# Performance work log

Hardware: AMD Instinct MI355X
Metric: run time of the kernel (lower is better)

Reference implementation:

```python
import math
import jax, jax.numpy as jnp
import numpy as np

PATCH_NUMS = (1, 2, 3, 4, 5, 6, 8, 10, 13, 16)
_lens = [p * p for p in PATCH_NUMS]
_cum = np.concatenate([[0], np.cumsum(_lens)])
BEGIN_ENDS = [(int(_cum[i]), int(_cum[i + 1])) for i in range(len(PATCH_NUMS))]
L_TOTAL = int(_cum[-1])  # 680

B, C = 32, 1024
S, P, M, R, NCAT = 10, 8, 4, 8, 22
SLOTS = P * M  # 32 slots per scale
MEM_RANK = 64
ALPHA_HID = 128


def setup_inputs() -> dict:
    key = jax.random.key(0)
    ks = jax.random.split(key, 24)
    inp = {}
    inp['x'] = jax.random.normal(ks[0], (B, L_TOTAL, C), jnp.float32)
    # -1 means CFG-unconditional sample (no category memory)
    inp['category_ids'] = jax.random.randint(ks[1], (B,), -1, NCAT)
    # shared memory, orthogonal-ish init rescaled to xavier std sqrt(2/(C+C))
    inp['shared_memory'] = jax.random.normal(ks[2], (S, SLOTS, C)) * math.sqrt(1.0 / C)
    inp['cat_A'] = jax.random.normal(ks[3], (NCAT, S, R)) * 0.01
    inp['cat_B'] = jax.random.normal(ks[4], (S, R, SLOTS * C)) * (1.0 / math.sqrt(R))
    inp['cat_emb'] = jax.random.normal(ks[5], (NCAT, C)) * 0.02
    inp['scale_emb'] = jax.random.normal(ks[6], (S, C)) * 0.02
    inp['Wq'] = jax.random.normal(ks[7], (C, C)) * (1.0 / math.sqrt(C))
    inp['Wk'] = jax.random.normal(ks[8], (C, C)) * (1.0 / math.sqrt(C))
    inp['Wv'] = jax.random.normal(ks[9], (C, C)) * (1.0 / math.sqrt(C))
    inp['aW1'] = jax.random.normal(ks[10], (3 * C, ALPHA_HID)) * (1.0 / math.sqrt(3 * C))
    inp['ab1'] = jnp.zeros((ALPHA_HID,), jnp.float32)
    inp['aW2'] = jax.random.normal(ks[11], (ALPHA_HID, 1)) * 0.01  # init zeros in torch; small random to exercise math
    inp['ab2'] = jnp.full((1,), -1.0, jnp.float32)
    inp['kW1'] = jax.random.normal(ks[12], (C, MEM_RANK)) * (1.0 / math.sqrt(C))
    inp['kb1'] = jnp.zeros((MEM_RANK,), jnp.float32)
    inp['kW2'] = jax.random.normal(ks[13], (MEM_RANK, C)) * (1.0 / math.sqrt(MEM_RANK))
    inp['kb2'] = jnp.zeros((C,), jnp.float32)
    inp['vW1'] = jax.random.normal(ks[14], (C, MEM_RANK)) * (1.0 / math.sqrt(C))
    inp['vb1'] = jnp.zeros((MEM_RANK,), jnp.float32)
    inp['vW2'] = jax.random.normal(ks[15], (MEM_RANK, C)) * (1.0 / math.sqrt(MEM_RANK))
    inp['vb2'] = jnp.zeros((C,), jnp.float32)
    inp['gk_logit'] = jnp.float32(-2.0)  # block_idx=0, depth=16
    inp['gv_logit'] = jnp.float32(-2.0)
    inp['log_temp'] = jnp.float32(math.log(0.1))
    return inp


def reference(x, category_ids, shared_memory, cat_A, cat_B, cat_emb, scale_emb,
              Wq, Wk, Wv, aW1, ab1, aW2, ab2,
              kW1, kb1, kW2, kb2, vW1, vb1, vW2, vb2,
              gk_logit, gv_logit, log_temp):
    Bb, L, Cc = x.shape
    temp = jnp.clip(jnp.exp(log_temp), 0.05, 1.0)
    inv_sqrt_c = 1.0 / math.sqrt(Cc)

    query = x @ Wq                              # [B, L, C]
    shared_k = shared_memory @ Wk               # [S, slots, C]
    shared_v = shared_memory @ Wv

    valid = (category_ids >= 0)                 # [B]
    cid = jnp.clip(category_ids, 0, None)
    a_all = cat_A[cid]                          # [B, S, R]
    ce = cat_emb[cid]                           # [B, C]

    outs = []
    for i, (s, e) in enumerate(BEGIN_ENDS):
        q = query[:, s:e, :]                    # [B, Ls, C]
        Ls = e - s
        V = i + 1                               # visible scales
        # --- shared retrieval over visible slots ---
        ks_ = shared_k[:V].reshape(V * SLOTS, Cc)
        vs_ = shared_v[:V].reshape(V * SLOTS, Cc)
        attn_s = jax.nn.softmax((q @ ks_.T) * inv_sqrt_c / temp, axis=-1)
        o_s = attn_s @ vs_                      # [B, Ls, C]
        # --- per-category memory: shared + low-rank residual ---
        delta = jnp.einsum('bvr,vrd->bvd', a_all[:, :V], cat_B[:V])
        delta = delta.reshape(Bb, V, SLOTS, Cc)
        cat_mem = (shared_memory[:V][None] + delta).reshape(Bb, V * SLOTS, Cc)
        kc = cat_mem @ Wk                       # [B, Vs, C]
        vc = cat_mem @ Wv
        attn_c = jax.nn.softmax(jnp.einsum('bld,bsd->bls', q, kc) * inv_sqrt_c / temp, axis=-1)
        o_c = jnp.einsum('bls,bsd->bld', attn_c, vc)
        # --- learned alpha blend (zeroed for invalid / CFG categories) ---
        ai = jnp.concatenate([
            q,
            jnp.broadcast_to(ce[:, None, :], (Bb, Ls, Cc)),
            jnp.broadcast_to(scale_emb[i][None, None, :], (Bb, Ls, Cc)),
        ], axis=-1)                             # [B, Ls, 3C]
        h = jax.nn.gelu(ai @ aW1 + ab1, approximate=False)
        alpha = jax.nn.sigmoid(h @ aW2 + ab2)   # [B, Ls, 1]
        alpha = jnp.where(valid[:, None, None], alpha, 0.0)
        outs.append(o_s + alpha * (o_c - o_s))

    mem = jnp.concatenate(outs, axis=1)         # [B, L, C]
    mem_k = jax.nn.sigmoid(gk_logit) * ((mem @ kW1 + kb1) @ kW2 + kb2)
    mem_v = jax.nn.sigmoid(gv_logit) * ((mem @ vW1 + vb1) @ vW2 + vb2)
    zero = jnp.float32(0.0)
    return mem_k, mem_v, zero, zero
```

## Files before the change

### kernel.cpp

```cpp
#include <hip/hip_runtime.h>
#include <math.h>

#define NB 32
#define NC 1024
#define LTOT 680

typedef unsigned short u16;
typedef __bf16 bf16x8 __attribute__((ext_vector_type(8)));
typedef float floatx4 __attribute__((ext_vector_type(4)));

__device__ __forceinline__ u16 f2bf(float f)
{
    union { float f; unsigned u; } v; v.f = f;
    unsigned u = v.u;
    u += 0x7FFFu + ((u >> 16) & 1u);
    return (u16)(u >> 16);
}

__device__ __forceinline__ float bf2f(unsigned u)
{
    union { unsigned u; float f; } v; v.u = u << 16; return v.f;
}

__device__ __forceinline__ void gload16(const u16* g, u16* l)
{
    typedef __attribute__((address_space(1))) const void gv_t;
    typedef __attribute__((address_space(3))) void lv_t;
    __builtin_amdgcn_global_load_lds(
        (gv_t*)(unsigned long long)(const void*)g,
        (lv_t*)(unsigned int)(unsigned long long)(void*)l,
        16, 0, 0);
}

__device__ __forceinline__ void slot_decode(int s, int* prow, int* pcq)
{
    *prow = ((s >> 7) << 4) | (s & 15);
    *pcq  = (((s >> 6) & 1) << 2) | ((s >> 4) & 3);
}

#define WAIT_VM8()  asm volatile("s_waitcnt vmcnt(8)" ::: "memory")
#define WAIT_VM0()  asm volatile("s_waitcnt vmcnt(0)" ::: "memory")
#define BAR()       __builtin_amdgcn_s_barrier()
#define SCHEDB()    __builtin_amdgcn_sched_barrier(0)

template<int OUTBF>
__global__ __launch_bounds__(256) void gemm_mfma(
    const u16* __restrict__ A, const u16* __restrict__ BT,
    float* __restrict__ C, int M, int N, int K, int lda,
    const float* __restrict__ bias, const float* __restrict__ scale_logit)
{
    __shared__ __align__(16) u16 As[2][8192];
    __shared__ __align__(16) u16 Bs[2][8192];

    const int tid  = threadIdx.x;
    const int m0   = blockIdx.y << 7;
    const int n0   = blockIdx.x << 7;
    const int wave = tid >> 6;
    const int lane = tid & 63;
    const int mh   = wave & 1;
    const int nh   = wave >> 1;
    const int lbase = (wave << 6) * 8;

    const u16* aSrc[4];
    const u16* bSrc[4];
#pragma unroll
    for (int p = 0; p < 4; ++p) {
        int s = tid + (p << 8), row, cq;
        slot_decode(s, &row, &cq);
        int gr = m0 + row; if (gr > M - 1) gr = M - 1;
        aSrc[p] = A + (size_t)gr * lda + (cq << 3);
        int gn = n0 + row; if (gn > N - 1) gn = N - 1;
        bSrc[p] = BT + (size_t)gn * K + (cq << 3);
    }

    floatx4 acc[4][4];
#pragma unroll
    for (int i = 0; i < 4; ++i)
#pragma unroll
        for (int j = 0; j < 4; ++j) acc[i][j] = (floatx4){0.f, 0.f, 0.f, 0.f};

#pragma unroll
    for (int p = 0; p < 4; ++p) gload16(aSrc[p], &As[0][lbase + (p << 11)]);
#pragma unroll
    for (int p = 0; p < 4; ++p) gload16(bSrc[p], &Bs[0][lbase + (p << 11)]);

    const int nt = K >> 6;
    for (int t = 0; t < nt; ++t) {
        const int cur = t & 1;
        if (t + 1 < nt) {
            const int kk = (t + 1) << 6;
#pragma unroll
            for (int p = 0; p < 4; ++p) gload16(aSrc[p] + kk, &As[cur ^ 1][lbase + (p << 11)]);
#pragma unroll
            for (int p = 0; p < 4; ++p) gload16(bSrc[p] + kk, &Bs[cur ^ 1][lbase + (p << 11)]);
            WAIT_VM8();
        } else {
            WAIT_VM0();
        }
        BAR(); SCHEDB();
#pragma unroll
        for (int kh = 0; kh < 2; ++kh) {
            bf16x8 a[4], b[4];
#pragma unroll
            for (int i = 0; i < 4; ++i)
                a[i] = *(const bf16x8*)&As[cur][(((((mh << 2) + i) << 1) | kh) * 64 + lane) * 8];
#pragma unroll
            for (int j = 0; j < 4; ++j)
                b[j] = *(const bf16x8*)&Bs[cur][(((((nh << 2) + j) << 1) | kh) * 64 + lane) * 8];
#pragma unroll
            for (int i = 0; i < 4; ++i)
#pragma unroll
                for (int j = 0; j < 4; ++j)
                    acc[i][j] = __builtin_amdgcn_mfma_f32_16x16x32_bf16(a[i], b[j], acc[i][j], 0, 0, 0);
        }
        SCHEDB(); BAR();
    }

    float scale = 1.f;
    if (scale_logit) scale = 1.f / (1.f + __expf(-scale_logit[0]));
    const int col = lane & 15, rquad = lane >> 4;
#pragma unroll
    for (int i = 0; i < 4; ++i) {
#pragma unroll
        for (int j = 0; j < 4; ++j) {
#pragma unroll
            for (int r = 0; r < 4; ++r) {
                int gr = m0 + (mh << 6) + (i << 4) + (rquad << 2) + r;
                int gc = n0 + (nh << 6) + (j << 4) + col;
                if (gr < M && gc < N) {
                    float bb = bias ? bias[gc] : 0.f;
                    float val = scale * (acc[i][j][r] + bb);
                    if (OUTBF) ((u16*)C)[(size_t)gr * N + gc] = f2bf(val);
                    else       C[(size_t)gr * N + gc] = val;
                }
            }
        }
    }
}

__global__ __launch_bounds__(256) void gemm_logits(
    const u16* __restrict__ Q, const u16* __restrict__ skb,
    const u16* __restrict__ kcb, float* __restrict__ out)
{
    __shared__ __align__(16) u16 As[2][8192];
    __shared__ __align__(16) u16 Bs[2][8192];

    const int tid  = threadIdx.x;
    const int m0   = blockIdx.x << 7;
    const int n0   = blockIdx.y << 7;
    const int b    = blockIdx.z;
    const int wave = tid >> 6;
    const int lane = tid & 63;
    const int mh   = wave & 1;
    const int nh   = wave >> 1;
    const int lbase = (wave << 6) * 8;

    const u16* Ab = Q   + (size_t)b * 680 * 1024;
    const u16* KC = kcb + (size_t)b * 320 * 1024;

    const u16* aSrc[4];
    const u16* bSrc[4];
#pragma unroll
    for (int p = 0; p < 4; ++p) {
        int s = tid + (p << 8), row, cq;
        slot_decode(s, &row, &cq);
        int gr = m0 + row; if (gr > 679) gr = 679;
        aSrc[p] = Ab + (size_t)gr * 1024 + (cq << 3);
        int gn = n0 + row;
        bSrc[p] = ((gn < 320) ? (skb + (size_t)gn * 1024)
                              : (KC + (size_t)(gn - 320) * 1024)) + (cq << 3);
    }

    floatx4 acc[4][4];
#pragma unroll
    for (int i = 0; i < 4; ++i)
#pragma unroll
        for (int j = 0; j < 4; ++j) acc[i][j] = (floatx4){0.f, 0.f, 0.f, 0.f};

#pragma unroll
    for (int p = 0; p < 4; ++p) gload16(aSrc[p], &As[0][lbase + (p << 11)]);
#pragma unroll
    for (int p = 0; p < 4; ++p) gload16(bSrc[p], &Bs[0][lbase + (p << 11)]);

    for (int t = 0; t < 16; ++t) {
        const int cur = t & 1;
        if (t < 15) {
            const int kk = (t + 1) << 6;
#pragma unroll
            for (int p = 0; p < 4; ++p) gload16(aSrc[p] + kk, &As[cur ^ 1][lbase + (p << 11)]);
#pragma unroll
            for (int p = 0; p < 4; ++p) gload16(bSrc[p] + kk, &Bs[cur ^ 1][lbase + (p << 11)]);
            WAIT_VM8();
        } else {
            WAIT_VM0();
        }
        BAR(); SCHEDB();
#pragma unroll
        for (int kh = 0; kh < 2; ++kh) {
            bf16x8 a[4], bb[4];
#pragma unroll
            for (int i = 0; i < 4; ++i)
                a[i] = *(const bf16x8*)&As[cur][(((((mh << 2) + i) << 1) | kh) * 64 + lane) * 8];
#pragma unroll
            for (int j = 0; j < 4; ++j)
                bb[j] = *(const bf16x8*)&Bs[cur][(((((nh << 2) + j) << 1) | kh) * 64 + lane) * 8];
#pragma unroll
            for (int i = 0; i < 4; ++i)
#pragma unroll
                for (int j = 0; j < 4; ++j)
                    acc[i][j] = __builtin_amdgcn_mfma_f32_16x16x32_bf16(a[i], bb[j], acc[i][j], 0, 0, 0);
        }
        SCHEDB(); BAR();
    }

    const int col = lane & 15, rquad = lane >> 4;
#pragma unroll
    for (int i = 0; i < 4; ++i)
#pragma unroll
        for (int j = 0; j < 4; ++j)
#pragma unroll
            for (int r = 0; r < 4; ++r) {
                int gr = m0 + (mh << 6) + (i << 4) + (rquad << 2) + r;
                int gc = n0 + (nh << 6) + (j << 4) + col;
                if (gr < 680)
                    out[((size_t)b * 680 + gr) * 640 + gc] = acc[i][j][r];
            }
}

__global__ __launch_bounds__(256) void gemm_pv(
    const u16* __restrict__ P, const u16* __restrict__ svT,
    const u16* __restrict__ vcT, u16* __restrict__ out)
{
    __shared__ __align__(16) u16 As[2][8192];
    __shared__ __align__(16) u16 Bs[2][8192];

    const int tid  = threadIdx.x;
    const int m0   = blockIdx.x << 7;
    const int n0   = blockIdx.y << 7;
    const int b    = blockIdx.z;
    const int wave = tid >> 6;
    const int lane = tid & 63;
    const int mh   = wave & 1;
    const int nh   = wave >> 1;
    const int lbase = (wave << 6) * 8;

    const u16* aSrc[4];
    const u16* bSrcS[4];
    const u16* bSrcC[4];
#pragma unroll
    for (int p = 0; p < 4; ++p) {
        int s = tid + (p << 8), row, cq;
        slot_decode(s, &row, &cq);
        int gr = m0 + row; if (gr > 679) gr = 679;
        aSrc[p] = P + ((size_t)b * 680 + gr) * 1280 + (cq << 3);
        int gn = n0 + row;
        bSrcS[p] = svT + (size_t)gn * 320 + (cq << 3);
        bSrcC[p] = vcT + ((size_t)b * 1024 + gn) * 320 + (cq << 3);
    }

    floatx4 acc[4][4];
#pragma unroll
    for (int i = 0; i < 4; ++i)
#pragma unroll
        for (int j = 0; j < 4; ++j) acc[i][j] = (floatx4){0.f, 0.f, 0.f, 0.f};

#pragma unroll
    for (int p = 0; p < 4; ++p) gload16(aSrc[p], &As[0][lbase + (p << 11)]);
#pragma unroll
    for (int p = 0; p < 4; ++p) gload16(bSrcS[p], &Bs[0][lbase + (p << 11)]);

    for (int t = 0; t < 10; ++t) {
        const int cur = t & 1;
        if (t < 9) {
            const int tn = t + 1;
            const int kk = tn << 6;
#pragma unroll
            for (int p = 0; p < 4; ++p) gload16(aSrc[p] + kk, &As[cur ^ 1][lbase + (p << 11)]);
#pragma unroll
            for (int p = 0; p < 4; ++p) {
                const u16* bp = (tn < 5) ? (bSrcS[p] + kk) : (bSrcC[p] + ((tn - 5) << 6));
                gload16(bp, &Bs[cur ^ 1][lbase + (p << 11)]);
            }
            WAIT_VM8();
        } else {
            WAIT_VM0();
        }
        BAR(); SCHEDB();
#pragma unroll
        for (int kh = 0; kh < 2; ++kh) {
            bf16x8 a[4], bb[4];
#pragma unroll
            for (int i = 0; i < 4; ++i)
                a[i] = *(const bf16x8*)&As[cur][(((((mh << 2) + i) << 1) | kh) * 64 + lane) * 8];
#pragma unroll
            for (int j = 0; j < 4; ++j)
                bb[j] = *(const bf16x8*)&Bs[cur][(((((nh << 2) + j) << 1) | kh) * 64 + lane) * 8];
#pragma unroll
            for (int i = 0; i < 4; ++i)
#pragma unroll
                for (int j = 0; j < 4; ++j)
                    acc[i][j] = __builtin_amdgcn_mfma_f32_16x16x32_bf16(a[i], bb[j], acc[i][j], 0, 0, 0);
        }
        SCHEDB(); BAR();
    }

    const int col = lane & 15, rquad = lane >> 4;
#pragma unroll
    for (int i = 0; i < 4; ++i)
#pragma unroll
        for (int j = 0; j < 4; ++j)
#pragma unroll
            for (int r = 0; r < 4; ++r) {
                int gr = m0 + (mh << 6) + (i << 4) + (rquad << 2) + r;
                int gc = n0 + (nh << 6) + (j << 4) + col;
                if (gr < 680)
                    out[((size_t)b * 680 + gr) * 1024 + gc] = f2bf(acc[i][j][r]);
            }
}

__global__ __launch_bounds__(256) void gemm_halpha(
    const u16* __restrict__ Q, const u16* __restrict__ W,
    const float* __restrict__ ceW, const float* __restrict__ seW,
    const int* __restrict__ cat_ids, u16* __restrict__ h)
{
    __shared__ __align__(16) u16 As[2][8192];
    __shared__ __align__(16) u16 Bs[2][8192];

    const int tid  = threadIdx.x;
    const int m0   = blockIdx.x << 7;
    const int wave = tid >> 6;
    const int lane = tid & 63;
    const int mh   = wave & 1;
    const int nh   = wave >> 1;
    const int lbase = (wave << 6) * 8;

    const u16* aSrc[4];
    const u16* bSrc[4];
#pragma unroll
    for (int p = 0; p < 4; ++p) {
        int s = tid + (p << 8), row, cq;
        slot_decode(s, &row, &cq);
        aSrc[p] = Q + (size_t)(m0 + row) * 1024 + (cq << 3);
        bSrc[p] = W + (size_t)row * 1024 + (cq << 3);
    }

    floatx4 acc[4][4];
#pragma unroll
    for (int i = 0; i < 4; ++i)
#pragma unroll
        for (int j = 0; j < 4; ++j) acc[i][j] = (floatx4){0.f, 0.f, 0.f, 0.f};

#pragma unroll
    for (int p = 0; p < 4; ++p) gload16(aSrc[p], &As[0][lbase + (p << 11)]);
#pragma unroll
    for (int p = 0; p < 4; ++p) gload16(bSrc[p], &Bs[0][lbase + (p << 11)]);

    for (int t = 0; t < 16; ++t) {
        const int cur = t & 1;
        if (t < 15) {
            const int kk = (t + 1) << 6;
#pragma unroll
            for (int p = 0; p < 4; ++p) gload16(aSrc[p] + kk, &As[cur ^ 1][lbase + (p << 11)]);
#pragma unroll
            for (int p = 0; p < 4; ++p) gload16(bSrc[p] + kk, &Bs[cur ^ 1][lbase + (p << 11)]);
            WAIT_VM8();
        } else {
            WAIT_VM0();
        }
        BAR(); SCHEDB();
#pragma unroll
        for (int kh = 0; kh < 2; ++kh) {
            bf16x8 a[4], bb[4];
#pragma unroll
            for (int i = 0; i < 4; ++i)
                a[i] = *(const bf16x8*)&As[cur][(((((mh << 2) + i) << 1) | kh) * 64 + lane) * 8];
#pragma unroll
            for (int j = 0; j < 4; ++j)
                bb[j] = *(const bf16x8*)&Bs[cur][(((((nh << 2) + j) << 1) | kh) * 64 + lane) * 8];
#pragma unroll
            for (int i = 0; i < 4; ++i)
#pragma unroll
                for (int j = 0; j < 4; ++j)
                    acc[i][j] = __builtin_amdgcn_mfma_f32_16x16x32_bf16(a[i], bb[j], acc[i][j], 0, 0, 0);
        }
        SCHEDB(); BAR();
    }

    const int se_[9] = {1,5,14,30,55,91,155,255,424};
    const int col = lane & 15, rquad = lane >> 4;
#pragma unroll
    for (int i = 0; i < 4; ++i) {
#pragma unroll
        for (int r = 0; r < 4; ++r) {
            int gr = m0 + (mh << 6) + (i << 4) + (rquad << 2) + r;
            int b  = gr / 680;
            int l  = gr - b * 680;
            int isc = 0;
#pragma unroll
            for (int k = 0; k < 9; ++k) if (l >= se_[k]) isc = k + 1;
            int cid = cat_ids[b]; if (cid < 0) cid = 0;
            const float* cw = ceW + cid * 128;
            const float* sw = seW + isc * 128;
#pragma unroll
            for (int j = 0; j < 4; ++j) {
                int gc = (nh << 6) + (j << 4) + col;
                float val = acc[i][j][r] + cw[gc] + sw[gc];
                float g = 0.5f * val * (1.0f + erff(val * 0.70710678118654752f));
                h[(size_t)gr * 128 + gc] = f2bf(g);
            }
        }
    }
}

__global__ __launch_bounds__(256) void alpha_reduce(
    const u16* __restrict__ h, const float* __restrict__ aW2,
    const float* __restrict__ ab2, const int* __restrict__ cat_ids,
    float* __restrict__ alpha)
{
    const int wave = threadIdx.x >> 6;
    const int lane = threadIdx.x & 63;
    const int row  = (blockIdx.x << 2) + wave;

    const unsigned pk = *(const unsigned*)(h + (size_t)row * 128 + (lane << 1));
    float s = bf2f(pk) * aW2[lane << 1] + bf2f(pk >> 16) * aW2[(lane << 1) + 1];
#pragma unroll
    for (int k = 32; k >= 1; k >>= 1) s += __shfl_xor(s, k);
    if (lane == 0) {
        int b = row / 680;
        float al = 0.f;
        if (cat_ids[b] >= 0) al = 1.f / (1.f + expf(-(s + ab2[0])));
        alpha[row] = al;
    }
}

__global__ __launch_bounds__(256) void softmax_kernel(
    float* __restrict__ logits, const float* __restrict__ alpha,
    const float* __restrict__ log_temp)
{
    const int tid  = threadIdx.x;
    const int w    = tid >> 6;
    const int lane = tid & 63;
    const int b    = blockIdx.y;
    const int l    = (blockIdx.x << 2) + w;

    const int se[10] = {1,5,14,30,55,91,155,255,424,680};
    int isc = 0;
#pragma unroll
    for (int k = 0; k < 9; ++k) if (l >= se[k]) isc = k + 1;
    const int NK = (isc + 1) << 5;

    float temp = __expf(log_temp[0]);
    temp = fminf(fmaxf(temp, 0.05f), 1.0f);
    const float Ksc = 0.03125f / temp;

    float* row = logits + ((size_t)b * 680 + l) * 640;

    float ls[5], lc[5];
#pragma unroll
    for (int u = 0; u < 5; ++u) {
        int j = lane + (u << 6);
        bool v = j < NK;
        ls[u] = v ? row[j]       : -1e30f;
        lc[u] = v ? row[320 + j] : -1e30f;
    }
    float mxs = -1e30f, mxc = -1e30f;
#pragma unroll
    for (int u = 0; u < 5; ++u) { mxs = fmaxf(mxs, ls[u]); mxc = fmaxf(mxc, lc[u]); }
#pragma unroll
    for (int k = 32; k >= 1; k >>= 1) {
        mxs = fmaxf(mxs, __shfl_xor(mxs, k));
        mxc = fmaxf(mxc, __shfl_xor(mxc, k));
    }
    float es[5], ec[5], ss = 0.f, sc = 0.f;
#pragma unroll
    for (int u = 0; u < 5; ++u) {
        int j = lane + (u << 6);
        bool v = j < NK;
        es[u] = v ? __expf((ls[u] - mxs) * Ksc) : 0.f;
        ec[u] = v ? __expf((lc[u] - mxc) * Ksc) : 0.f;
        ss += es[u]; sc += ec[u];
    }
#pragma unroll
    for (int k = 32; k >= 1; k >>= 1) {
        ss += __shfl_xor(ss, k);
        sc += __shfl_xor(sc, k);
    }
    const float al = alpha[b * LTOT + l];
    const float wS = (1.f - al) / ss;
    const float wC = al / sc;

    u16* po = (u16*)row;
#pragma unroll
    for (int u = 0; u < 5; ++u) {
        int j = lane + (u << 6);
        po[j]       = f2bf(es[u] * wS);
        po[320 + j] = f2bf(ec[u] * wC);
    }
}

__global__ __launch_bounds__(256) void castbf(
    const float* __restrict__ in, u16* __restrict__ out, int n4)
{
    int i = blockIdx.x * 256 + threadIdx.x;
    const int stride = gridDim.x * 256;
    for (; i < n4; i += stride) {
        const float4 v = ((const float4*)in)[i];
        uint2 o;
        o.x = (unsigned)f2bf(v.x) | ((unsigned)f2bf(v.y) << 16);
        o.y = (unsigned)f2bf(v.z) | ((unsigned)f2bf(v.w) << 16);
        ((uint2*)out)[i] = o;
    }
}

__global__ __launch_bounds__(256) void tcast(
    const float* __restrict__ in, u16* __restrict__ out, int R, int Cc)
{
    __shared__ float t[32][33];
    const int bx = blockIdx.x * 32;
    const int by = blockIdx.y * 32;
    const int x = threadIdx.x & 31;
    const int y0 = threadIdx.x >> 5;
#pragma unroll
    for (int yy = y0; yy < 32; yy += 8)
        t[yy][x] = (by + yy < R && bx + x < Cc)
                 ? in[(size_t)(by + yy) * Cc + bx + x] : 0.f;
    __syncthreads();
#pragma unroll
    for (int yy = y0; yy < 32; yy += 8)
        if (bx + yy < Cc && by + x < R)
            out[(size_t)(bx + yy) * R + by + x] = f2bf(t[x][yy]);
}

__global__ __launch_bounds__(256) void transpose32(
    const float* __restrict__ in, float* __restrict__ out, int R, int Cc)
{
    __shared__ float t[32][33];
    const int bx = blockIdx.x * 32;
    const int by = blockIdx.y * 32;
    const int x = threadIdx.x & 31;
    const int y0 = threadIdx.x >> 5;
#pragma unroll
    for (int yy = y0; yy < 32; yy += 8)
        t[yy][x] = (by + yy < R && bx + x < Cc)
                 ? in[(size_t)(by + yy) * Cc + bx + x] : 0.f;
    __syncthreads();
#pragma unroll
    for (int yy = y0; yy < 32; yy += 8)
        if (bx + yy < Cc && by + x < R)
            out[(size_t)(bx + yy) * R + by + x] = t[x][yy];
}

__global__ __launch_bounds__(256) void build_kc(
    const float* __restrict__ sk, const float* __restrict__ catBK,
    const float* __restrict__ cat_A, const int* __restrict__ cat_ids,
    u16* __restrict__ kc)
{
    const int b = blockIdx.x;
    const int jrow = blockIdx.y;
    const int v = jrow >> 5, slot = jrow & 31;
    int cid = cat_ids[b]; if (cid < 0) cid = 0;
    float a[8];
#pragma unroll
    for (int r = 0; r < 8; ++r) a[r] = cat_A[(cid * 10 + v) * 8 + r];
    const int c = threadIdx.x << 2;
    float4 acc = *(const float4*)(sk + (size_t)jrow * 1024 + c);
#pragma unroll
    for (int r = 0; r < 8; ++r) {
        const float4 bv = *(const float4*)(catBK + (size_t)((v * 8 + r) * 32 + slot) * 1024 + c);
        acc.x = fmaf(a[r], bv.x, acc.x);
        acc.y = fmaf(a[r], bv.y, acc.y);
        acc.z = fmaf(a[r], bv.z, acc.z);
        acc.w = fmaf(a[r], bv.w, acc.w);
    }
    uint2 pk;
    pk.x = (unsigned)f2bf(acc.x) | ((unsigned)f2bf(acc.y) << 16);
    pk.y = (unsigned)f2bf(acc.z) | ((unsigned)f2bf(acc.w) << 16);
    *(uint2*)(kc + ((size_t)b * 320 + jrow) * 1024 + c) = pk;
}

__global__ __launch_bounds__(320) void build_vcT(
    const float* __restrict__ svT, const float* __restrict__ catBVT,
    const float* __restrict__ cat_A, const int* __restrict__ cat_ids,
    u16* __restrict__ vcT)
{
    __shared__ float aS[80];
    const int b = blockIdx.x;
    const int c = blockIdx.y;
    const int tid = threadIdx.x;
    if (tid < 80) {
        int cid = cat_ids[b]; if (cid < 0) cid = 0;
        aS[tid] = cat_A[cid * 80 + tid];
    }
    __syncthreads();
    const int j = tid;
    const int v = j >> 5, slot = j & 31;
    float acc = svT[(size_t)c * 320 + j];
    const float* row = catBVT + (size_t)c * 2560;
#pragma unroll
    for (int r = 0; r < 8; ++r)
        acc = fmaf(aS[v * 8 + r], row[(v * 8 + r) * 32 + slot], acc);
    vcT[((size_t)b * 1024 + c) * 320 + j] = f2bf(acc);
}

__global__ void concat_bias(const float* __restrict__ a,
                            const float* __restrict__ b, float* __restrict__ o)
{
    int t = threadIdx.x;
    if (t < 64) o[t] = a[t];
    else if (t < 128) o[t] = b[t - 64];
}

__global__ void tail_zero(float* p)
{
    if (threadIdx.x < 2) p[threadIdx.x] = 0.f;
}

extern "C" void kernel_launch(void* const* d_in, const int* in_sizes, int n_in,
                              void* d_out, int out_size, void* d_ws, size_t ws_size,
                              hipStream_t stream)
{
    (void)in_sizes; (void)n_in;
    const float* x         = (const float*)d_in[0];
    const int*   cat_ids   = (const int*)  d_in[1];
    const float* sm        = (const float*)d_in[2];
    const float* cat_A     = (const float*)d_in[3];
    const float* cat_B     = (const float*)d_in[4];
    const float* cat_emb   = (const float*)d_in[5];
    const float* scale_emb = (const float*)d_in[6];
    const float* Wq        = (const float*)d_in[7];
    const float* Wk        = (const float*)d_in[8];
    const float* Wv        = (const float*)d_in[9];
    const float* aW1       = (const float*)d_in[10];
    const float* ab1       = (const float*)d_in[11];
    const float* aW2       = (const float*)d_in[12];
    const float* ab2       = (const float*)d_in[13];
    const float* kW1       = (const float*)d_in[14];
    const float* kb1       = (const float*)d_in[15];
    const float* kW2       = (const float*)d_in[16];
    const float* kb2       = (const float*)d_in[17];
    const float* vW1       = (const float*)d_in[18];
    const float* vb1       = (const float*)d_in[19];
    const float* vW2       = (const float*)d_in[20];
    const float* vb2       = (const float*)d_in[21];
    const float* gk        = (const float*)d_in[22];
    const float* gv        = (const float*)d_in[23];
    const float* log_temp  = (const float*)d_in[24];

    float* out   = (float*)d_out;
    float* memb  = out;
    float* outv  = out + (size_t)21760 * 1024;

    float* w      = (float*)d_ws;
    u16*   kc_bf  = (u16*)w;
    u16*   vcT_bf = (u16*)(w + 5242880);
    float* sk     = w + 10485760;
    float* sv     = w + 10813440;
    float* svT    = w + 11141120;
    u16*   sk_bf  = (u16*)(w + 11468800);
    u16*   svT_bf = (u16*)(w + 11632640);
    float* alph   = w + 11796480;
    float* logits = w + 11859200;
    float* tail0  = w + 25785600;
    u16*   aW1topT = (u16*)tail0;
    u16*   aW1midT = (u16*)(tail0 + 65536);
    u16*   aW1botT = (u16*)(tail0 + 131072);
    float* ceW    = tail0 + 196608;
    float* seW    = tail0 + 199424;
    float* cb     = tail0 + 200704;
    u16*   h_bf   = (u16*)(tail0 + 200832);
    u16*   catB_bf = (u16*)(w + 27379072);
    u16*   sm_bf  = (u16*)(w + 28689792);
    u16*   ce_bf  = (u16*)(w + 28853632);
    u16*   se_bf  = (u16*)(w + 28864896);
    if (ws_size < (size_t)29881600 * 4) return;
    if (out_size < 2 * 21760 * 1024 + 2) return;

    u16*   x_bf   = (u16*)logits;
    float* bufA   = logits + 5570560;
    float* bufB   = bufA + 2621440;
    float* catBVT = bufB + 2621440;
    u16*   WqT    = (u16*)w;
    u16*   WkT    = WqT + 1048576;
    u16*   WvT    = WkT + 1048576;
    u16*   kW1T   = (u16*)sv;
    u16*   vW1T   = kW1T + 65536;
    u16*   kW2T   = vW1T + 65536;
    u16*   vW2T   = kW2T + 65536;
    u16*   bufAB_bf = (u16*)w;
    u16*   mem_bf = (u16*)memb;
    u16*   query_bf = (u16*)outv;

    const dim3 blk256(256);

    castbf<<<dim3(2048), blk256, 0, stream>>>(x, x_bf, 21760 * 1024 / 4);
    castbf<<<dim3(320), blk256, 0, stream>>>(sm, sm_bf, 320 * 1024 / 4);
    castbf<<<dim3(2048), blk256, 0, stream>>>(cat_B, catB_bf, 2560 * 1024 / 4);
    castbf<<<dim3(22), blk256, 0, stream>>>(cat_emb, ce_bf, 22 * 1024 / 4);
    castbf<<<dim3(10), blk256, 0, stream>>>(scale_emb, se_bf, 10 * 1024 / 4);
    tcast<<<dim3(32, 32), blk256, 0, stream>>>(Wq, WqT, 1024, 1024);
    tcast<<<dim3(32, 32), blk256, 0, stream>>>(Wk, WkT, 1024, 1024);
    tcast<<<dim3(32, 32), blk256, 0, stream>>>(Wv, WvT, 1024, 1024);
    tcast<<<dim3(4, 32), blk256, 0, stream>>>(aW1,              aW1topT, 1024, 128);
    tcast<<<dim3(4, 32), blk256, 0, stream>>>(aW1 + 1024 * 128, aW1midT, 1024, 128);
    tcast<<<dim3(4, 32), blk256, 0, stream>>>(aW1 + 2048 * 128, aW1botT, 1024, 128);

    gemm_mfma<1><<<dim3(8, 170), blk256, 0, stream>>>(x_bf,    WqT, (float*)query_bf, 21760, 1024, 1024, 1024, nullptr, nullptr);
    gemm_mfma<0><<<dim3(8, 3),   blk256, 0, stream>>>(sm_bf,   WkT, sk,   320,  1024, 1024, 1024, nullptr, nullptr);
    gemm_mfma<0><<<dim3(8, 3),   blk256, 0, stream>>>(sm_bf,   WvT, sv,   320,  1024, 1024, 1024, nullptr, nullptr);
    gemm_mfma<0><<<dim3(8, 20),  blk256, 0, stream>>>(catB_bf, WkT, bufA, 2560, 1024, 1024, 1024, nullptr, nullptr);
    gemm_mfma<0><<<dim3(8, 20),  blk256, 0, stream>>>(catB_bf, WvT, bufB, 2560, 1024, 1024, 1024, nullptr, nullptr);

    gemm_mfma<0><<<dim3(1, 1), blk256, 0, stream>>>(ce_bf, aW1midT, ceW, 22, 128, 1024, 1024, nullptr, nullptr);
    gemm_mfma<0><<<dim3(1, 1), blk256, 0, stream>>>(se_bf, aW1botT, seW, 10, 128, 1024, 1024, ab1, nullptr);

    castbf<<<dim3(320), blk256, 0, stream>>>(sk, sk_bf, 320 * 1024 / 4);
    transpose32<<<dim3(32, 10), blk256, 0, stream>>>(sv, svT, 320, 1024);
    tcast<<<dim3(32, 10), blk256, 0, stream>>>(sv, svT_bf, 320, 1024);
    transpose32<<<dim3(32, 80), blk256, 0, stream>>>(bufB, catBVT, 2560, 1024);
    tcast<<<dim3(2, 32), blk256, 0, stream>>>(kW1, kW1T, 1024, 64);
    tcast<<<dim3(2, 32), blk256, 0, stream>>>(vW1, vW1T, 1024, 64);
    tcast<<<dim3(32, 2), blk256, 0, stream>>>(kW2, kW2T, 64, 1024);
    tcast<<<dim3(32, 2), blk256, 0, stream>>>(vW2, vW2T, 64, 1024);
    concat_bias<<<dim3(1), dim3(128), 0, stream>>>(kb1, vb1, cb);

    build_kc<<<dim3(NB, 320), blk256, 0, stream>>>(sk, bufA, cat_A, cat_ids, kc_bf);
    build_vcT<<<dim3(NB, 1024), dim3(320), 0, stream>>>(svT, catBVT, cat_A, cat_ids, vcT_bf);

    gemm_halpha<<<dim3(170), blk256, 0, stream>>>(query_bf, aW1topT, ceW, seW, cat_ids, h_bf);
    alpha_reduce<<<dim3(5440), blk256, 0, stream>>>(h_bf, aW2, ab2, cat_ids, alph);

    gemm_logits<<<dim3(6, 5, NB), blk256, 0, stream>>>(query_bf, sk_bf, kc_bf, logits);
    softmax_kernel<<<dim3(170, NB), blk256, 0, stream>>>(logits, alph, log_temp);
    gemm_pv<<<dim3(6, 8, NB), blk256, 0, stream>>>((const u16*)logits, svT_bf, vcT_bf, mem_bf);

    gemm_mfma<1><<<dim3(1, 170), blk256, 0, stream>>>(mem_bf, kW1T, (float*)bufAB_bf, 21760, 128, 1024, 1024, cb, nullptr);
    gemm_mfma<0><<<dim3(8, 170), blk256, 0, stream>>>(bufAB_bf,      kW2T, memb, 21760, 1024, 64, 128, kb2, gk);
    gemm_mfma<0><<<dim3(8, 170), blk256, 0, stream>>>(bufAB_bf + 64, vW2T, outv, 21760, 1024, 64, 128, vb2, gv);

    tail_zero<<<1, 64, 0, stream>>>(out + (size_t)2 * 21760 * 1024);
}
```

Measured before the change: 922.2 us.

## Use 256x256 tiles with 512-thread GEMMs and batch-amortized memory builders

Replaces the 128x128, 256-thread MFMA GEMMs for the large projections, logits and PV products with 256x256 tiles, 8 waves and a K-step of 32. This raises arithmetic intensity per loaded byte. The build_kc/build_vcT kernels now stage the catB rows in shared memory once and loop over all 32 batches, so the rows are not re-read per batch. In exchange, the larger tiles give fewer blocks (worse wave quantization, e.g. 3x3 logits tiles with padding) and more accumulator registers, and the shorter K-step means more barriers per unit of work.

Result: slower. 993.3 us (+7.7%).

```diff
diff --git a/kernel.cpp b/kernel.cpp
--- a/kernel.cpp
+++ b/kernel.cpp
@@ -38,10 +38,289 @@
     *pcq  = (((s >> 6) & 1) << 2) | ((s >> 4) & 3);
 }
 
+__device__ __forceinline__ void slot_decode256(int s, int* prow, int* pcq)
+{
+    *prow = ((s >> 6) << 4) | (s & 15);
+    *pcq  = (s >> 4) & 3;
+}
+
 #define WAIT_VM8()  asm volatile("s_waitcnt vmcnt(8)" ::: "memory")
+#define WAIT_VM4()  asm volatile("s_waitcnt vmcnt(4)" ::: "memory")
 #define WAIT_VM0()  asm volatile("s_waitcnt vmcnt(0)" ::: "memory")
 #define BAR()       __builtin_amdgcn_s_barrier()
 #define SCHEDB()    __builtin_amdgcn_sched_barrier(0)
+
+template<int OUTBF>
+__global__ __launch_bounds__(512) void gemm256(
+    const u16* __restrict__ A, const u16* __restrict__ BT,
+    float* __restrict__ C, int M, int N, int K, int lda,
+    const float* __restrict__ bias, const float* __restrict__ scale_logit)
+{
+    __shared__ __align__(16) u16 As[2][8192];
+    __shared__ __align__(16) u16 Bs[2][8192];
+
+    const int tid  = threadIdx.x;
+    const int m0   = blockIdx.y << 8;
+    const int n0   = blockIdx.x << 8;
+    const int wave = tid >> 6;
+    const int lane = tid & 63;
+    const int mh   = wave & 1;
+    const int nh   = wave >> 1;
+    const int lbase = (wave << 6) * 8;
+
+    const u16* aSrc[2];
+    const u16* bSrc[2];
+#pragma unroll
+    for (int p = 0; p < 2; ++p) {
+        int s = tid + (p << 9), row, cq;
+        slot_decode256(s, &row, &cq);
+        int gr = m0 + row; if (gr > M - 1) gr = M - 1;
+        aSrc[p] = A + (size_t)gr * lda + (cq << 3);
+        int gn = n0 + row; if (gn > N - 1) gn = N - 1;
+        bSrc[p] = BT + (size_t)gn * K + (cq << 3);
+    }
+
+    floatx4 acc[8][4];
+#pragma unroll
+    for (int i = 0; i < 8; ++i)
+#pragma unroll
+        for (int j = 0; j < 4; ++j) acc[i][j] = (floatx4){0.f, 0.f, 0.f, 0.f};
+
+#pragma unroll
+    for (int p = 0; p < 2; ++p) gload16(aSrc[p], &As[0][lbase + (p << 12)]);
+#pragma unroll
+    for (int p = 0; p < 2; ++p) gload16(bSrc[p], &Bs[0][lbase + (p << 12)]);
+
+    const int nt = K >> 5;
+    for (int t = 0; t < nt; ++t) {
+        const int cur = t & 1;
+        if (t + 1 < nt) {
+            const int kk = (t + 1) << 5;
+#pragma unroll
+            for (int p = 0; p < 2; ++p) gload16(aSrc[p] + kk, &As[cur ^ 1][lbase + (p << 12)]);
+#pragma unroll
+            for (int p = 0; p < 2; ++p) gload16(bSrc[p] + kk, &Bs[cur ^ 1][lbase + (p << 12)]);
+            WAIT_VM4();
+        } else {
+            WAIT_VM0();
+        }
+        BAR(); SCHEDB();
+        {
+            bf16x8 a[8], b[4];
+#pragma unroll
+            for (int i = 0; i < 8; ++i)
+                a[i] = *(const bf16x8*)&As[cur][((((mh << 3) + i) << 6) + lane) * 8];
+#pragma unroll
+            for (int j = 0; j < 4; ++j)
+                b[j] = *(const bf16x8*)&Bs[cur][((((nh << 2) + j) << 6) + lane) * 8];
+#pragma unroll
+            for (int i = 0; i < 8; ++i)
+#pragma unroll
+                for (int j = 0; j < 4; ++j)
+                    acc[i][j] = __builtin_amdgcn_mfma_f32_16x16x32_bf16(a[i], b[j], acc[i][j], 0, 0, 0);
+        }
+        SCHEDB(); BAR();
+    }
+
+    float scale = 1.f;
+    if (scale_logit) scale = 1.f / (1.f + __expf(-scale_logit[0]));
+    const int col = lane & 15, rquad = lane >> 4;
+#pragma unroll
+    for (int i = 0; i < 8; ++i) {
+#pragma unroll
+        for (int j = 0; j < 4; ++j) {
+#pragma unroll
+            for (int r = 0; r < 4; ++r) {
+                int gr = m0 + (mh << 7) + (i << 4) + (rquad << 2) + r;
+                int gc = n0 + (nh << 6) + (j << 4) + col;
+                if (gr < M && gc < N) {
+                    float bb = bias ? bias[gc] : 0.f;
+                    float val = scale * (acc[i][j][r] + bb);
+                    if (OUTBF) ((u16*)C)[(size_t)gr * N + gc] = f2bf(val);
+                    else       C[(size_t)gr * N + gc] = val;
+                }
+            }
+        }
+    }
+}
+
+__global__ __launch_bounds__(512) void gemm256_logits(
+    const u16* __restrict__ Q, const u16* __restrict__ skb,
+    const u16* __restrict__ kcb, float* __restrict__ out)
+{
+    __shared__ __align__(16) u16 As[2][8192];
+    __shared__ __align__(16) u16 Bs[2][8192];
+
+    const int tid  = threadIdx.x;
+    const int m0   = blockIdx.y << 8;
+    const int n0   = blockIdx.x << 8;
+    const int b    = blockIdx.z;
+    const int wave = tid >> 6;
+    const int lane = tid & 63;
+    const int mh   = wave & 1;
+    const int nh   = wave >> 1;
+    const int lbase = (wave << 6) * 8;
+
+    const u16* Ab = Q   + (size_t)b * 680 * 1024;
+    const u16* KC = kcb + (size_t)b * 320 * 1024;
+
+    const u16* aSrc[2];
+    const u16* bSrc[2];
+#pragma unroll
+    for (int p = 0; p < 2; ++p) {
+        int s = tid + (p << 9), row, cq;
+        slot_decode256(s, &row, &cq);
+        int gr = m0 + row; if (gr > 679) gr = 679;
+        aSrc[p] = Ab + (size_t)gr * 1024 + (cq << 3);
+        int gn = n0 + row; if (gn > 639) gn = 639;
+        bSrc[p] = ((gn < 320) ? (skb + (size_t)gn * 1024)
+                              : (KC + (size_t)(gn - 320) * 1024)) + (cq << 3);
+    }
+
+    floatx4 acc[8][4];
+#pragma unroll
+    for (int i = 0; i < 8; ++i)
+#pragma unroll
+        for (int j = 0; j < 4; ++j) acc[i][j] = (floatx4){0.f, 0.f, 0.f, 0.f};
+
+#pragma unroll
+    for (int p = 0; p < 2; ++p) gload16(aSrc[p], &As[0][lbase + (p << 12)]);
+#pragma unroll
+    for (int p = 0; p < 2; ++p) gload16(bSrc[p], &Bs[0][lbase + (p << 12)]);
+
+    for (int t = 0; t < 32; ++t) {
+        const int cur = t & 1;
+        if (t < 31) {
+            const int kk = (t + 1) << 5;
+#pragma unroll
+            for (int p = 0; p < 2; ++p) gload16(aSrc[p] + kk, &As[cur ^ 1][lbase + (p << 12)]);
+#pragma unroll
+            for (int p = 0; p < 2; ++p) gload16(bSrc[p] + kk, &Bs[cur ^ 1][lbase + (p << 12)]);
+            WAIT_VM4();
+        } else {
+            WAIT_VM0();
+        }
+        BAR(); SCHEDB();
+        {
+            bf16x8 a[8], bb[4];
+#pragma unroll
+            for (int i = 0; i < 8; ++i)
+                a[i] = *(const bf16x8*)&As[cur][((((mh << 3) + i) << 6) + lane) * 8];
+#pragma unroll
+            for (int j = 0; j < 4; ++j)
+                bb[j] = *(const bf16x8*)&Bs[cur][((((nh << 2) + j) << 6) + lane) * 8];
+#pragma unroll
+            for (int i = 0; i < 8; ++i)
+#pragma unroll
+                for (int j = 0; j < 4; ++j)
+                    acc[i][j] = __builtin_amdgcn_mfma_f32_16x16x32_bf16(a[i], bb[j], acc[i][j], 0, 0, 0);
+        }
+        SCHEDB(); BAR();
+    }
+
+    const int col = lane & 15, rquad = lane >> 4;
+#pragma unroll
+    for (int i = 0; i < 8; ++i)
+#pragma unroll
+        for (int j = 0; j < 4; ++j)
+#pragma unroll
+            for (int r = 0; r < 4; ++r) {
+                int gr = m0 + (mh << 7) + (i << 4) + (rquad << 2) + r;
+                int gc = n0 + (nh << 6) + (j << 4) + col;
+                if (gr < 680 && gc < 640)
+                    out[((size_t)b * 680 + gr) * 640 + gc] = acc[i][j][r];
+            }
+}
+
+__global__ __launch_bounds__(512) void gemm256_pv(
+    const u16* __restrict__ P, const u16* __restrict__ svT,
+    const u16* __restrict__ vcT, u16* __restrict__ out)
+{
+    __shared__ __align__(16) u16 As[2][8192];
+    __shared__ __align__(16) u16 Bs[2][8192];
+
+    const int tid  = threadIdx.x;
+    const int m0   = blockIdx.y << 8;
+    const int n0   = blockIdx.x << 8;
+    const int b    = blockIdx.z;
+    const int wave = tid >> 6;
+    const int lane = tid & 63;
+    const int mh   = wave & 1;
+    const int nh   = wave >> 1;
+    const int lbase = (wave << 6) * 8;
+
+    const u16* aSrc[2];
+    const u16* bSrcS[2];
+    const u16* bSrcC[2];
+#pragma unroll
+    for (int p = 0; p < 2; ++p) {
+        int s = tid + (p << 9), row, cq;
+        slot_decode256(s, &row, &cq);
+        int gr = m0 + row; if (gr > 679) gr = 679;
+        aSrc[p] = P + ((size_t)b * 680 + gr) * 1280 + (cq << 3);
+        int gn = n0 + row;
+        bSrcS[p] = svT + (size_t)gn * 320 + (cq << 3);
+        bSrcC[p] = vcT + ((size_t)b * 1024 + gn) * 320 + (cq << 3);
+    }
+
+    floatx4 acc[8][4];
+#pragma unroll
+    for (int i = 0; i < 8; ++i)
+#pragma unroll
+        for (int j = 0; j < 4; ++j) acc[i][j] = (floatx4){0.f, 0.f, 0.f, 0.f};
+
+#pragma unroll
+    for (int p = 0; p < 2; ++p) gload16(aSrc[p], &As[0][lbase + (p << 12)]);
+#pragma unroll
+    for (int p = 0; p < 2; ++p) gload16(bSrcS[p], &Bs[0][lbase + (p << 12)]);
+
+    for (int t = 0; t < 20; ++t) {
+        const int cur = t & 1;
+        if (t < 19) {
+            const int tn = t + 1;
+            const int kk = tn << 5;
+#pragma unroll
+            for (int p = 0; p < 2; ++p) gload16(aSrc[p] + kk, &As[cur ^ 1][lbase + (p << 12)]);
+#pragma unroll
+            for (int p = 0; p < 2; ++p) {
+                const u16* bp = (tn < 10) ? (bSrcS[p] + kk) : (bSrcC[p] + ((tn - 10) << 5));
+                gload16(bp, &Bs[cur ^ 1][lbase + (p << 12)]);
+            }
+            WAIT_VM4();
+        } else {
+            WAIT_VM0();
+        }
+        BAR(); SCHEDB();
+        {
+            bf16x8 a[8], bb[4];
+#pragma unroll
+            for (int i = 0; i < 8; ++i)
+                a[i] = *(const bf16x8*)&As[cur][((((mh << 3) + i) << 6) + lane) * 8];
+#pragma unroll
+            for (int j = 0; j < 4; ++j)
+                bb[j] = *(const bf16x8*)&Bs[cur][((((nh << 2) + j) << 6) + lane) * 8];
+#pragma unroll
+            for (int i = 0; i < 8; ++i)
+#pragma unroll
+                for (int j = 0; j < 4; ++j)
+                    acc[i][j] = __builtin_amdgcn_mfma_f32_16x16x32_bf16(a[i], bb[j], acc[i][j], 0, 0, 0);
+        }
+        SCHEDB(); BAR();
+    }
+
+    const int col = lane & 15, rquad = lane >> 4;
+#pragma unroll
+    for (int i = 0; i < 8; ++i)
+#pragma unroll
+        for (int j = 0; j < 4; ++j)
+#pragma unroll
+            for (int r = 0; r < 4; ++r) {
+                int gr = m0 + (mh << 7) + (i << 4) + (rquad << 2) + r;
+                int gc = n0 + (nh << 6) + (j << 4) + col;
+                if (gr < 680)
+                    out[((size_t)b * 680 + gr) * 1024 + gc] = f2bf(acc[i][j][r]);
+            }
+}
 
 template<int OUTBF>
 __global__ __launch_bounds__(256) void gemm_mfma(
@@ -138,186 +417,6 @@
     }
 }
 
-__global__ __launch_bounds__(256) void gemm_logits(
-    const u16* __restrict__ Q, const u16* __restrict__ skb,
-    const u16* __restrict__ kcb, float* __restrict__ out)
-{
-    __shared__ __align__(16) u16 As[2][8192];
-    __shared__ __align__(16) u16 Bs[2][8192];
-
-    const int tid  = threadIdx.x;
-    const int m0   = blockIdx.x << 7;
-    const int n0   = blockIdx.y << 7;
-    const int b    = blockIdx.z;
-    const int wave = tid >> 6;
-    const int lane = tid & 63;
-    const int mh   = wave & 1;
-    const int nh   = wave >> 1;
-    const int lbase = (wave << 6) * 8;
-
-    const u16* Ab = Q   + (size_t)b * 680 * 1024;
-    const u16* KC = kcb + (size_t)b * 320 * 1024;
-
-    const u16* aSrc[4];
-    const u16* bSrc[4];
-#pragma unroll
-    for (int p = 0; p < 4; ++p) {
-        int s = tid + (p << 8), row, cq;
-        slot_decode(s, &row, &cq);
-        int gr = m0 + row; if (gr > 679) gr = 679;
-        aSrc[p] = Ab + (size_t)gr * 1024 + (cq << 3);
-        int gn = n0 + row;
-        bSrc[p] = ((gn < 320) ? (skb + (size_t)gn * 1024)
-                              : (KC + (size_t)(gn - 320) * 1024)) + (cq << 3);
-    }
-
-    floatx4 acc[4][4];
-#pragma unroll
-    for (int i = 0; i < 4; ++i)
-#pragma unroll
-        for (int j = 0; j < 4; ++j) acc[i][j] = (floatx4){0.f, 0.f, 0.f, 0.f};
-
-#pragma unroll
-    for (int p = 0; p < 4; ++p) gload16(aSrc[p], &As[0][lbase + (p << 11)]);
-#pragma unroll
-    for (int p = 0; p < 4; ++p) gload16(bSrc[p], &Bs[0][lbase + (p << 11)]);
-
-    for (int t = 0; t < 16; ++t) {
-        const int cur = t & 1;
-        if (t < 15) {
-            const int kk = (t + 1) << 6;
-#pragma unroll
-            for (int p = 0; p < 4; ++p) gload16(aSrc[p] + kk, &As[cur ^ 1][lbase + (p << 11)]);
-#pragma unroll
-            for (int p = 0; p < 4; ++p) gload16(bSrc[p] + kk, &Bs[cur ^ 1][lbase + (p << 11)]);
-            WAIT_VM8();
-        } else {
-            WAIT_VM0();
-        }
-        BAR(); SCHEDB();
-#pragma unroll
-        for (int kh = 0; kh < 2; ++kh) {
-            bf16x8 a[4], bb[4];
-#pragma unroll
-            for (int i = 0; i < 4; ++i)
-                a[i] = *(const bf16x8*)&As[cur][(((((mh << 2) + i) << 1) | kh) * 64 + lane) * 8];
-#pragma unroll
-            for (int j = 0; j < 4; ++j)
-                bb[j] = *(const bf16x8*)&Bs[cur][(((((nh << 2) + j) << 1) | kh) * 64 + lane) * 8];
-#pragma unroll
-            for (int i = 0; i < 4; ++i)
-#pragma unroll
-                for (int j = 0; j < 4; ++j)
-                    acc[i][j] = __builtin_amdgcn_mfma_f32_16x16x32_bf16(a[i], bb[j], acc[i][j], 0, 0, 0);
-        }
-        SCHEDB(); BAR();
-    }
-
-    const int col = lane & 15, rquad = lane >> 4;
-#pragma unroll
-    for (int i = 0; i < 4; ++i)
-#pragma unroll
-        for (int j = 0; j < 4; ++j)
-#pragma unroll
-            for (int r = 0; r < 4; ++r) {
-                int gr = m0 + (mh << 6) + (i << 4) + (rquad << 2) + r;
-                int gc = n0 + (nh << 6) + (j << 4) + col;
-                if (gr < 680)
-                    out[((size_t)b * 680 + gr) * 640 + gc] = acc[i][j][r];
-            }
-}
-
-__global__ __launch_bounds__(256) void gemm_pv(
-    const u16* __restrict__ P, const u16* __restrict__ svT,
-    const u16* __restrict__ vcT, u16* __restrict__ out)
-{
-    __shared__ __align__(16) u16 As[2][8192];
-    __shared__ __align__(16) u16 Bs[2][8192];
-
-    const int tid  = threadIdx.x;
-    const int m0   = blockIdx.x << 7;
-    const int n0   = blockIdx.y << 7;
-    const int b    = blockIdx.z;
-    const int wave = tid >> 6;
-    const int lane = tid & 63;
-    const int mh   = wave & 1;
-    const int nh   = wave >> 1;
-    const int lbase = (wave << 6) * 8;
-
-    const u16* aSrc[4];
-    const u16* bSrcS[4];
-    const u16* bSrcC[4];
-#pragma unroll
-    for (int p = 0; p < 4; ++p) {
-        int s = tid + (p << 8), row, cq;
-        slot_decode(s, &row, &cq);
-        int gr = m0 + row; if (gr > 679) gr = 679;
-        aSrc[p] = P + ((size_t)b * 680 + gr) * 1280 + (cq << 3);
-        int gn = n0 + row;
-        bSrcS[p] = svT + (size_t)gn * 320 + (cq << 3);
-        bSrcC[p] = vcT + ((size_t)b * 1024 + gn) * 320 + (cq << 3);
-    }
-
-    floatx4 acc[4][4];
-#pragma unroll
-    for (int i = 0; i < 4; ++i)
-#pragma unroll
-        for (int j = 0; j < 4; ++j) acc[i][j] = (floatx4){0.f, 0.f, 0.f, 0.f};
-
-#pragma unroll
-    for (int p = 0; p < 4; ++p) gload16(aSrc[p], &As[0][lbase + (p << 11)]);
-#pragma unroll
-    for (int p = 0; p < 4; ++p) gload16(bSrcS[p], &Bs[0][lbase + (p << 11)]);
-
-    for (int t = 0; t < 10; ++t) {
-        const int cur = t & 1;
-        if (t < 9) {
-            const int tn = t + 1;
-            const int kk = tn << 6;
-#pragma unroll
-            for (int p = 0; p < 4; ++p) gload16(aSrc[p] + kk, &As[cur ^ 1][lbase + (p << 11)]);
-#pragma unroll
-            for (int p = 0; p < 4; ++p) {
-                const u16* bp = (tn < 5) ? (bSrcS[p] + kk) : (bSrcC[p] + ((tn - 5) << 6));
-                gload16(bp, &Bs[cur ^ 1][lbase + (p << 11)]);
-            }
-            WAIT_VM8();
-        } else {
-            WAIT_VM0();
-        }
-        BAR(); SCHEDB();
-#pragma unroll
-        for (int kh = 0; kh < 2; ++kh) {
-            bf16x8 a[4], bb[4];
-#pragma unroll
-            for (int i = 0; i < 4; ++i)
-                a[i] = *(const bf16x8*)&As[cur][(((((mh << 2) + i) << 1) | kh) * 64 + lane) * 8];
-#pragma unroll
-            for (int j = 0; j < 4; ++j)
-                bb[j] = *(const bf16x8*)&Bs[cur][(((((nh << 2) + j) << 1) | kh) * 64 + lane) * 8];
-#pragma unroll
-            for (int i = 0; i < 4; ++i)
-#pragma unroll
-                for (int j = 0; j < 4; ++j)
-                    acc[i][j] = __builtin_amdgcn_mfma_f32_16x16x32_bf16(a[i], bb[j], acc[i][j], 0, 0, 0);
-        }
-        SCHEDB(); BAR();
-    }
-
-    const int col = lane & 15, rquad = lane >> 4;
-#pragma unroll
-    for (int i = 0; i < 4; ++i)
-#pragma unroll
-        for (int j = 0; j < 4; ++j)
-#pragma unroll
-            for (int r = 0; r < 4; ++r) {
-                int gr = m0 + (mh << 6) + (i << 4) + (rquad << 2) + r;
-                int gc = n0 + (nh << 6) + (j << 4) + col;
-                if (gr < 680)
-                    out[((size_t)b * 680 + gr) * 1024 + gc] = f2bf(acc[i][j][r]);
-            }
-}
-
 __global__ __launch_bounds__(256) void gemm_halpha(
     const u16* __restrict__ Q, const u16* __restrict__ W,
     const float* __restrict__ ceW, const float* __restrict__ seW,
@@ -550,56 +649,83 @@
             out[(size_t)(bx + yy) * R + by + x] = t[x][yy];
 }
 
-__global__ __launch_bounds__(256) void build_kc(
+__global__ __launch_bounds__(256) void build_kc2(
     const float* __restrict__ sk, const float* __restrict__ catBK,
     const float* __restrict__ cat_A, const int* __restrict__ cat_ids,
     u16* __restrict__ kc)
 {
-    const int b = blockIdx.x;
-    const int jrow = blockIdx.y;
+    __shared__ float bk[8][1024];
+    __shared__ float skr[1024];
+    __shared__ float aS[32][8];
+    const int jrow = blockIdx.x;
     const int v = jrow >> 5, slot = jrow & 31;
-    int cid = cat_ids[b]; if (cid < 0) cid = 0;
-    float a[8];
-#pragma unroll
-    for (int r = 0; r < 8; ++r) a[r] = cat_A[(cid * 10 + v) * 8 + r];
-    const int c = threadIdx.x << 2;
-    float4 acc = *(const float4*)(sk + (size_t)jrow * 1024 + c);
-#pragma unroll
-    for (int r = 0; r < 8; ++r) {
-        const float4 bv = *(const float4*)(catBK + (size_t)((v * 8 + r) * 32 + slot) * 1024 + c);
-        acc.x = fmaf(a[r], bv.x, acc.x);
-        acc.y = fmaf(a[r], bv.y, acc.y);
-        acc.z = fmaf(a[r], bv.z, acc.z);
-        acc.w = fmaf(a[r], bv.w, acc.w);
-    }
-    uint2 pk;
-    pk.x = (unsigned)f2bf(acc.x) | ((unsigned)f2bf(acc.y) << 16);
-    pk.y = (unsigned)f2bf(acc.z) | ((unsigned)f2bf(acc.w) << 16);
-    *(uint2*)(kc + ((size_t)b * 320 + jrow) * 1024 + c) = pk;
-}
-
-__global__ __launch_bounds__(320) void build_vcT(
+    const int tid = threadIdx.x;
+
+    for (int idx = tid; idx < 2048; idx += 256) {
+        int r = idx >> 8, c4 = (idx & 255) << 2;
+        *(float4*)&bk[r][c4] =
+            *(const float4*)(catBK + (size_t)((v * 8 + r) * 32 + slot) * 1024 + c4);
+    }
+    *(float4*)&skr[tid << 2] = *(const float4*)(sk + (size_t)jrow * 1024 + (tid << 2));
+    {
+        int b = tid >> 3, r = tid & 7;
+        int cid = cat_ids[b]; if (cid < 0) cid = 0;
+        aS[b][r] = cat_A[(cid * 10 + v) * 8 + r];
+    }
+    __syncthreads();
+
+    const int c = tid << 2;
+    const float4 base = *(const float4*)&skr[c];
+    for (int b = 0; b < 32; ++b) {
+        float4 acc = base;
+#pragma unroll
+        for (int r = 0; r < 8; ++r) {
+            const float a = aS[b][r];
+            const float4 bv = *(const float4*)&bk[r][c];
+            acc.x = fmaf(a, bv.x, acc.x);
+            acc.y = fmaf(a, bv.y, acc.y);
+            acc.z = fmaf(a, bv.z, acc.z);
+            acc.w = fmaf(a, bv.w, acc.w);
+        }
+        uint2 pk;
+        pk.x = (unsigned)f2bf(acc.x) | ((unsigned)f2bf(acc.y) << 16);
+        pk.y = (unsigned)f2bf(acc.z) | ((unsigned)f2bf(acc.w) << 16);
+        *(uint2*)(kc + ((size_t)b * 320 + jrow) * 1024 + c) = pk;
+    }
+}
+
+__global__ __launch_bounds__(320) void build_vcT2(
     const float* __restrict__ svT, const float* __restrict__ catBVT,
     const float* __restrict__ cat_A, const int* __restrict__ cat_ids,
     u16* __restrict__ vcT)
 {
-    __shared__ float aS[80];
-    const int b = blockIdx.x;
-    const int c = blockIdx.y;
+    __shared__ float rowS[2560];
+    __shared__ float svr[320];
+    __shared__ float aS[32][80];
+    const int c = blockIdx.x;
     const int tid = threadIdx.x;
-    if (tid < 80) {
+
+    for (int idx = tid; idx < 2560; idx += 320)
+        rowS[idx] = catBVT[(size_t)c * 2560 + idx];
+    svr[tid] = svT[(size_t)c * 320 + tid];
+    for (int idx = tid; idx < 2560; idx += 320) {
+        int b = idx / 80, t = idx - b * 80;
         int cid = cat_ids[b]; if (cid < 0) cid = 0;
-        aS[tid] = cat_A[cid * 80 + tid];
+        aS[b][t] = cat_A[cid * 80 + t];
     }
     __syncthreads();
-    const int j = tid;
-    const int v = j >> 5, slot = j & 31;
-    float acc = svT[(size_t)c * 320 + j];
-    const float* row = catBVT + (size_t)c * 2560;
-#pragma unroll
-    for (int r = 0; r < 8; ++r)
-        acc = fmaf(aS[v * 8 + r], row[(v * 8 + r) * 32 + slot], acc);
-    vcT[((size_t)b * 1024 + c) * 320 + j] = f2bf(acc);
+
+    const int j = tid, v = j >> 5, slot = j & 31;
+    const float base = svr[j];
+    const float* rp = &rowS[v * 256 + slot];
+    for (int b = 0; b < 32; ++b) {
+        float acc = base;
+        const float* ap = &aS[b][v * 8];
+#pragma unroll
+        for (int r = 0; r < 8; ++r)
+            acc = fmaf(ap[r], rp[r * 32], acc);
+        vcT[((size_t)b * 1024 + c) * 320 + j] = f2bf(acc);
+    }
 }
 
 __global__ void concat_bias(const float* __restrict__ a,
@@ -691,6 +817,7 @@
     u16*   query_bf = (u16*)outv;
 
     const dim3 blk256(256);
+    const dim3 blk512(512);
 
     castbf<<<dim3(2048), blk256, 0, stream>>>(x, x_bf, 21760 * 1024 / 4);
     castbf<<<dim3(320), blk256, 0, stream>>>(sm, sm_bf, 320 * 1024 / 4);
@@ -704,11 +831,11 @@
     tcast<<<dim3(4, 32), blk256, 0, stream>>>(aW1 + 1024 * 128, aW1midT, 1024, 128);
     tcast<<<dim3(4, 32), blk256, 0, stream>>>(aW1 + 2048 * 128, aW1botT, 1024, 128);
 
-    gemm_mfma<1><<<dim3(8, 170), blk256, 0, stream>>>(x_bf,    WqT, (float*)query_bf, 21760, 1024, 1024, 1024, nullptr, nullptr);
-    gemm_mfma<0><<<dim3(8, 3),   blk256, 0, stream>>>(sm_bf,   WkT, sk,   320,  1024, 1024, 1024, nullptr, nullptr);
-    gemm_mfma<0><<<dim3(8, 3),   blk256, 0, stream>>>(sm_bf,   WvT, sv,   320,  1024, 1024, 1024, nullptr, nullptr);
-    gemm_mfma<0><<<dim3(8, 20),  blk256, 0, stream>>>(catB_bf, WkT, bufA, 2560, 1024, 1024, 1024, nullptr, nullptr);
-    gemm_mfma<0><<<dim3(8, 20),  blk256, 0, stream>>>(catB_bf, WvT, bufB, 2560, 1024, 1024, 1024, nullptr, nullptr);
+    gemm256<1><<<dim3(4, 85), blk512, 0, stream>>>(x_bf,    WqT, (float*)query_bf, 21760, 1024, 1024, 1024, nullptr, nullptr);
+    gemm256<0><<<dim3(4, 2),  blk512, 0, stream>>>(sm_bf,   WkT, sk,   320,  1024, 1024, 1024, nullptr, nullptr);
+    gemm256<0><<<dim3(4, 2),  blk512, 0, stream>>>(sm_bf,   WvT, sv,   320,  1024, 1024, 1024, nullptr, nullptr);
+    gemm256<0><<<dim3(4, 10), blk512, 0, stream>>>(catB_bf, WkT, bufA, 2560, 1024, 1024, 1024, nullptr, nullptr);
+    gemm256<0><<<dim3(4, 10), blk512, 0, stream>>>(catB_bf, WvT, bufB, 2560, 1024, 1024, 1024, nullptr, nullptr);
 
     gemm_mfma<0><<<dim3(1, 1), blk256, 0, stream>>>(ce_bf, aW1midT, ceW, 22, 128, 1024, 1024, nullptr, nullptr);
     gemm_mfma<0><<<dim3(1, 1), blk256, 0, stream>>>(se_bf, aW1botT, seW, 10, 128, 1024, 1024, ab1, nullptr);
@@ -723,19 +850,19 @@
     tcast<<<dim3(32, 2), blk256, 0, stream>>>(vW2, vW2T, 64, 1024);
     concat_bias<<<dim3(1), dim3(128), 0, stream>>>(kb1, vb1, cb);
 
-    build_kc<<<dim3(NB, 320), blk256, 0, stream>>>(sk, bufA, cat_A, cat_ids, kc_bf);
-    build_vcT<<<dim3(NB, 1024), dim3(320), 0, stream>>>(svT, catBVT, cat_A, cat_ids, vcT_bf);
+    build_kc2<<<dim3(320), blk256, 0, stream>>>(sk, bufA, cat_A, cat_ids, kc_bf);
+    build_vcT2<<<dim3(1024), dim3(320), 0, stream>>>(svT, catBVT, cat_A, cat_ids, vcT_bf);
 
     gemm_halpha<<<dim3(170), blk256, 0, stream>>>(query_bf, aW1topT, ceW, seW, cat_ids, h_bf);
     alpha_reduce<<<dim3(5440), blk256, 0, stream>>>(h_bf, aW2, ab2, cat_ids, alph);
 
-    gemm_logits<<<dim3(6, 5, NB), blk256, 0, stream>>>(query_bf, sk_bf, kc_bf, logits);
+    gemm256_logits<<<dim3(3, 3, NB), blk512, 0, stream>>>(query_bf, sk_bf, kc_bf, logits);
     softmax_kernel<<<dim3(170, NB), blk256, 0, stream>>>(logits, alph, log_temp);
-    gemm_pv<<<dim3(6, 8, NB), blk256, 0, stream>>>((const u16*)logits, svT_bf, vcT_bf, mem_bf);
+    gemm256_pv<<<dim3(4, 3, NB), blk512, 0, stream>>>((const u16*)logits, svT_bf, vcT_bf, mem_bf);
 
     gemm_mfma<1><<<dim3(1, 170), blk256, 0, stream>>>(mem_bf, kW1T, (float*)bufAB_bf, 21760, 128, 1024, 1024, cb, nullptr);
-    gemm_mfma<0><<<dim3(8, 170), blk256, 0, stream>>>(bufAB_bf,      kW2T, memb, 21760, 1024, 64, 128, kb2, gk);
-    gemm_mfma<0><<<dim3(8, 170), blk256, 0, stream>>>(bufAB_bf + 64, vW2T, outv, 21760, 1024, 64, 128, vb2, gv);
+    gemm256<0><<<dim3(4, 85), blk512, 0, stream>>>(bufAB_bf,      kW2T, memb, 21760, 1024, 64, 128, kb2, gk);
+    gemm256<0><<<dim3(4, 85), blk512, 0, stream>>>(bufAB_bf + 64, vW2T, outv, 21760, 1024, 64, 128, vb2, gv);
 
     tail_zero<<<1, 64, 0, stream>>>(out + (size_t)2 * 21760 * 1024);
 }
```
